# Optimization experiments

Measured on AMD Instinct MI355X. Metric: run time of the kernel, lower is better.

Reference implementation:

```python
import jax, jax.numpy as jnp
import numpy as np

N_EMBD = 1024
N_HEAD = 16

def setup_inputs() -> dict:
    key = jax.random.key(0)
    ks = jax.random.split(key, 5)
    B, T, C = 4, 2048, N_EMBD
    scale = 1.0 / np.sqrt(C)
    return {
        "x": jax.random.normal(ks[0], (B, T, C), dtype=jnp.float32),
        "w_qkv": jax.random.normal(ks[1], (C, 3 * C), dtype=jnp.float32) * scale,
        "b_qkv": jax.random.normal(ks[2], (3 * C,), dtype=jnp.float32) * 0.02,
        "w_proj": jax.random.normal(ks[3], (C, C), dtype=jnp.float32) * scale,
        "b_proj": jax.random.normal(ks[4], (C,), dtype=jnp.float32) * 0.02,
    }

def reference(x, w_qkv, b_qkv, w_proj, b_proj):
    B, T, C = x.shape
    H = N_HEAD
    D = C // H  # head dim
    qkv = x @ w_qkv + b_qkv  # [B,T,3C]
    q, k, v = jnp.split(qkv, 3, axis=-1)
    # [B,T,C] -> [B,H,T,D]
    q = q.reshape(B, T, H, D).transpose(0, 2, 1, 3)
    k = k.reshape(B, T, H, D).transpose(0, 2, 1, 3)
    v = v.reshape(B, T, H, D).transpose(0, 2, 1, 3)
    att = jnp.einsum("bhqd,bhkd->bhqk", q, k) / jnp.sqrt(jnp.asarray(D, x.dtype))
    causal = jnp.tril(jnp.ones((T, T), dtype=bool))  # [T,T]
    att = jnp.where(causal[None, None, :, :], att, -jnp.inf)
    att = jax.nn.softmax(att, axis=-1)
    y = jnp.einsum("bhqk,bhkd->bhqd", att, v)  # [B,H,T,D]
    y = y.transpose(0, 2, 1, 3).reshape(B, T, C)
    return y @ w_proj + b_proj
```

## Files before the change

### kernel.cpp

```cpp
#include <hip/hip_runtime.h>
#include <hip/hip_bf16.h>
#include <stdint.h>

typedef __bf16 bf16_8 __attribute__((ext_vector_type(8)));
typedef float f32_4 __attribute__((ext_vector_type(4)));
typedef short short4v __attribute__((ext_vector_type(4)));

#define VMCNT(n) asm volatile("s_waitcnt vmcnt(" #n ")" ::: "memory")
#define LGKM0 asm volatile("s_waitcnt lgkmcnt(0)" ::: "memory")
#define SBAR __builtin_amdgcn_s_barrier()
#define SCHB __builtin_amdgcn_sched_barrier(0)

static __device__ __forceinline__ unsigned short f2bf(float f) {
    union { float f; unsigned int u; } v; v.f = f;
    unsigned int u = v.u;
    unsigned int r = (u + 0x7fffu + ((u >> 16) & 1u)) >> 16;
    return (unsigned short)r;
}

static __device__ __forceinline__ unsigned int pack_bf16x2(float a, float b) {
    union { float f; unsigned int u; } ua, ub;
    ua.f = a; ub.f = b;
    return __builtin_amdgcn_perm(ub.u + 0x8000u, ua.u + 0x8000u, 0x07060302u);
}

static __device__ __forceinline__ f32_4 mfma_16x16x16_bf16(short4v a, short4v b, f32_4 c) {
#if __has_builtin(__builtin_amdgcn_mfma_f32_16x16x16bf16_1k)
    return __builtin_amdgcn_mfma_f32_16x16x16bf16_1k(a, b, c, 0, 0, 0);
#else
    asm volatile("v_mfma_f32_16x16x16_bf16 %0, %1, %2, %0"
                 : "+v"(c) : "v"(a), "v"(b));
    return c;
#endif
}

static __device__ __forceinline__ void gll16(const unsigned short* g, unsigned short* l) {
    __builtin_amdgcn_global_load_lds(
        (const __attribute__((address_space(1))) unsigned int*)g,
        (__attribute__((address_space(3))) unsigned int*)l, 16, 0, 0);
}

__global__ __launch_bounds__(256) void prep_kernel(
    const float* __restrict__ x, unsigned int* __restrict__ xbf,
    const float* __restrict__ w_qkv, unsigned short* __restrict__ wqkvt,
    const float* __restrict__ w_proj, unsigned short* __restrict__ wprojt) {
    __shared__ unsigned short tile[64][65];
    int bid = blockIdx.x;
    if (bid < 8192) {
        int i = bid * 256 + threadIdx.x;
        float4 f = ((const float4*)x)[i];
        uint2 o;
        o.x = pack_bf16x2(f.x, f.y);
        o.y = pack_bf16x2(f.z, f.w);
        ((uint2*)xbf)[i] = o;
        return;
    }
    const float* in; unsigned short* out; int N, bx, by;
    if (bid < 8960) {
        in = w_qkv; out = wqkvt; N = 3072;
        int t = bid - 8192; bx = t % 48; by = t / 48;
    } else {
        in = w_proj; out = wprojt; N = 1024;
        int t = bid - 8960; bx = t & 15; by = t >> 4;
    }
    const int K = 1024;
    int k0 = by * 64, n0 = bx * 64;
    int tc = threadIdx.x & 63, tr = threadIdx.x >> 6;
    for (int p = 0; p < 16; ++p) {
        int k = p * 4 + tr;
        tile[k][tc] = f2bf(in[(size_t)(k0 + k) * N + n0 + tc]);
    }
    __syncthreads();
    for (int p = 0; p < 16; ++p) {
        int n = p * 4 + tr;
        out[(size_t)(n0 + n) * K + k0 + tc] = tile[tc][n];
    }
}

#define QSCALE 0.1803368801111204f

__global__ __launch_bounds__(512) void gemm_qkv(
    const unsigned short* __restrict__ A,
    const unsigned short* __restrict__ Bt,
    const float* __restrict__ bias,
    int M, int N, int K,
    unsigned short* __restrict__ q_out, unsigned short* __restrict__ k_out,
    unsigned short* __restrict__ v_out) {
    __shared__ __align__(16) unsigned short As[3][256 * 64];
    __shared__ __align__(16) unsigned short Bs[3][128 * 64];
    int tid = threadIdx.x;
    int wave = tid >> 6, lane = tid & 63;
    int wm = wave >> 1, wn = wave & 1;
    int quad = lane >> 4, l16 = lane & 15;
    int m0 = blockIdx.y * 256, n0 = blockIdx.x * 128;
    int which = n0 >> 10;

    f32_4 acc[4][4] = {};

    int srow = lane >> 3;
    int scs = ((lane & 7) ^ srow) * 8;
    const unsigned short* Ag = A + (size_t)(m0 + wave * 32 + srow) * K + scs;
    const unsigned short* Bg = Bt + (size_t)(n0 + wave * 16 + srow) * K + scs;
    int sx = l16 & 7;

    unsigned short *a0 = As[0], *a1 = As[1], *a2 = As[2];
    unsigned short *b0 = Bs[0], *b1 = Bs[1], *b2 = Bs[2];

#define STG_A(dst, kc) do { \
        for (int g = 0; g < 4; ++g) \
            gll16(Ag + (kc) + (size_t)(g * 8) * K, (dst) + (wave * 32 + g * 8) * 64); \
    } while (0)
#define STG_B(dst, kc) do { \
        for (int g = 0; g < 2; ++g) \
            gll16(Bg + (kc) + (size_t)(g * 8) * K, (dst) + (wave * 16 + g * 8) * 64); \
    } while (0)

    STG_A(a0, 0); STG_B(b0, 0);
    STG_A(a1, 64); STG_B(b1, 64);

    const int nkt = K >> 6;
    for (int kt = 0; kt < nkt; ++kt) {
        if (kt + 1 < nkt) { VMCNT(6); } else { VMCNT(0); }
        SCHB; SBAR; SCHB;
        bf16_8 af[4], bfr[4];
        for (int i = 0; i < 4; ++i)
            af[i] = *(const bf16_8*)(a0 + (wm * 64 + i * 16 + l16) * 64 +
                                     ((unsigned)(quad ^ sx)) * 8);
        for (int j = 0; j < 4; ++j)
            bfr[j] = *(const bf16_8*)(b0 + (wn * 64 + j * 16 + l16) * 64 +
                                      ((unsigned)(quad ^ sx)) * 8);
        if (kt + 2 < nkt) STG_A(a2, (kt + 2) * 64);
        SCHB; SBAR; SCHB;
        LGKM0; SCHB;
        __builtin_amdgcn_s_setprio(1);
        if (which < 2) {
            for (int i = 0; i < 4; ++i)
                for (int j = 0; j < 4; ++j)
                    acc[i][j] = __builtin_amdgcn_mfma_f32_16x16x32_bf16(bfr[j], af[i], acc[i][j], 0, 0, 0);
        } else {
            for (int i = 0; i < 4; ++i)
                for (int j = 0; j < 4; ++j)
                    acc[i][j] = __builtin_amdgcn_mfma_f32_16x16x32_bf16(af[i], bfr[j], acc[i][j], 0, 0, 0);
        }
        __builtin_amdgcn_s_setprio(0);

        SCHB; SBAR; SCHB;
        for (int i = 0; i < 4; ++i)
            af[i] = *(const bf16_8*)(a0 + (wm * 64 + i * 16 + l16) * 64 +
                                     ((unsigned)((4 + quad) ^ sx)) * 8);
        for (int j = 0; j < 4; ++j)
            bfr[j] = *(const bf16_8*)(b0 + (wn * 64 + j * 16 + l16) * 64 +
                                      ((unsigned)((4 + quad) ^ sx)) * 8);
        if (kt + 2 < nkt) STG_B(b2, (kt + 2) * 64);
        SCHB; SBAR; SCHB;
        LGKM0; SCHB;
        __builtin_amdgcn_s_setprio(1);
        if (which < 2) {
            for (int i = 0; i < 4; ++i)
                for (int j = 0; j < 4; ++j)
                    acc[i][j] = __builtin_amdgcn_mfma_f32_16x16x32_bf16(bfr[j], af[i], acc[i][j], 0, 0, 0);
        } else {
            for (int i = 0; i < 4; ++i)
                for (int j = 0; j < 4; ++j)
                    acc[i][j] = __builtin_amdgcn_mfma_f32_16x16x32_bf16(af[i], bfr[j], acc[i][j], 0, 0, 0);
        }
        __builtin_amdgcn_s_setprio(0);

        unsigned short* t;
        t = a0; a0 = a1; a1 = a2; a2 = t;
        t = b0; b0 = b1; b1 = b2; b2 = t;
    }
#undef STG_A
#undef STG_B

    int b = m0 >> 11;
    int tbase = (m0 & 2047) + wm * 64;
    int nw0 = n0 + wn * 64;
    if (which < 2) {
        unsigned short* dst = which == 0 ? q_out : k_out;
        float scale = which == 0 ? QSCALE : 1.0f;
        int h0 = ((n0 & 1023) >> 6) + wn;
        size_t base = ((size_t)((b << 4) + h0) * 2048) * 64;
        for (int j = 0; j < 4; ++j) {
            float4 b4 = *(const float4*)(bias + nw0 + j * 16 + quad * 4);
            int d0 = j * 16 + quad * 4;
            for (int i = 0; i < 4; ++i) {
                int t = tbase + i * 16 + l16;
                uint2 pk;
                pk.x = pack_bf16x2((acc[i][j][0] + b4.x) * scale,
                                   (acc[i][j][1] + b4.y) * scale);
                pk.y = pack_bf16x2((acc[i][j][2] + b4.z) * scale,
                                   (acc[i][j][3] + b4.w) * scale);
                *(uint2*)(dst + base + (size_t)t * 64 + d0) = pk;
            }
        }
    } else {
        for (int j = 0; j < 4; ++j) {
            int n = nw0 + j * 16 + l16;
            int c = n & 1023, h = c >> 6, d = c & 63;
            float bs = bias[n];
            size_t base = ((size_t)((b << 4) + h) * 64 + d) * 2048;
            for (int i = 0; i < 4; ++i) {
                int t0 = tbase + i * 16 + quad * 4;
                uint2 pk;
                pk.x = pack_bf16x2(acc[i][j][0] + bs, acc[i][j][1] + bs);
                pk.y = pack_bf16x2(acc[i][j][2] + bs, acc[i][j][3] + bs);
                *(uint2*)(v_out + base + t0) = pk;
            }
        }
    }
}

__global__ __launch_bounds__(512) void gemm_proj(
    const unsigned short* __restrict__ A,
    const unsigned short* __restrict__ Bt,
    const float* __restrict__ bias,
    int M, int N, int K, float* __restrict__ outf) {
    __shared__ __align__(16) unsigned short As[3][256 * 64];
    __shared__ __align__(16) unsigned short Bs[3][128 * 64];
    int tid = threadIdx.x;
    int wave = tid >> 6, lane = tid & 63;
    int wm = wave >> 1, wn = wave & 1;
    int quad = lane >> 4, l16 = lane & 15;
    int m0 = blockIdx.y * 256, n0 = blockIdx.x * 128;

    f32_4 acc[4][4] = {};

    int srow = lane >> 3;
    int scs = ((lane & 7) ^ srow) * 8;
    const unsigned short* Ag = A + (size_t)(m0 + wave * 32 + srow) * K + scs;
    const unsigned short* Bg = Bt + (size_t)(n0 + wave * 16 + srow) * K + scs;
    int sx = l16 & 7;

    unsigned short *a0 = As[0], *a1 = As[1], *a2 = As[2];
    unsigned short *b0 = Bs[0], *b1 = Bs[1], *b2 = Bs[2];

#define STG_A(dst, kc) do { \
        for (int g = 0; g < 4; ++g) \
            gll16(Ag + (kc) + (size_t)(g * 8) * K, (dst) + (wave * 32 + g * 8) * 64); \
    } while (0)
#define STG_B(dst, kc) do { \
        for (int g = 0; g < 2; ++g) \
            gll16(Bg + (kc) + (size_t)(g * 8) * K, (dst) + (wave * 16 + g * 8) * 64); \
    } while (0)

    STG_A(a0, 0); STG_B(b0, 0);
    STG_A(a1, 64); STG_B(b1, 64);

    const int nkt = K >> 6;
    for (int kt = 0; kt < nkt; ++kt) {
        if (kt + 1 < nkt) { VMCNT(6); } else { VMCNT(0); }
        SCHB; SBAR; SCHB;
        bf16_8 af[4], bfr[4];
        for (int i = 0; i < 4; ++i)
            af[i] = *(const bf16_8*)(a0 + (wm * 64 + i * 16 + l16) * 64 +
                                     ((unsigned)(quad ^ sx)) * 8);
        for (int j = 0; j < 4; ++j)
            bfr[j] = *(const bf16_8*)(b0 + (wn * 64 + j * 16 + l16) * 64 +
                                      ((unsigned)(quad ^ sx)) * 8);
        if (kt + 2 < nkt) STG_A(a2, (kt + 2) * 64);
        SCHB; SBAR; SCHB;
        LGKM0; SCHB;
        __builtin_amdgcn_s_setprio(1);
        for (int i = 0; i < 4; ++i)
            for (int j = 0; j < 4; ++j)
                acc[i][j] = __builtin_amdgcn_mfma_f32_16x16x32_bf16(af[i], bfr[j], acc[i][j], 0, 0, 0);
        __builtin_amdgcn_s_setprio(0);

        SCHB; SBAR; SCHB;
        for (int i = 0; i < 4; ++i)
            af[i] = *(const bf16_8*)(a0 + (wm * 64 + i * 16 + l16) * 64 +
                                     ((unsigned)((4 + quad) ^ sx)) * 8);
        for (int j = 0; j < 4; ++j)
            bfr[j] = *(const bf16_8*)(b0 + (wn * 64 + j * 16 + l16) * 64 +
                                      ((unsigned)((4 + quad) ^ sx)) * 8);
        if (kt + 2 < nkt) STG_B(b2, (kt + 2) * 64);
        SCHB; SBAR; SCHB;
        LGKM0; SCHB;
        __builtin_amdgcn_s_setprio(1);
        for (int i = 0; i < 4; ++i)
            for (int j = 0; j < 4; ++j)
                acc[i][j] = __builtin_amdgcn_mfma_f32_16x16x32_bf16(af[i], bfr[j], acc[i][j], 0, 0, 0);
        __builtin_amdgcn_s_setprio(0);

        unsigned short* t;
        t = a0; a0 = a1; a1 = a2; a2 = t;
        t = b0; b0 = b1; b1 = b2; b2 = t;
    }
#undef STG_A
#undef STG_B

    for (int j = 0; j < 4; ++j) {
        int n = n0 + wn * 64 + j * 16 + l16;
        float bs = bias[n];
        for (int i = 0; i < 4; ++i) {
            int m = m0 + wm * 64 + i * 16 + quad * 4;
            for (int r = 0; r < 4; ++r)
                outf[(size_t)(m + r) * N + n] = acc[i][j][r] + bs;
        }
    }
}

__global__ __launch_bounds__(256, 5) void attn_kernel(
    const unsigned short* __restrict__ Q, const unsigned short* __restrict__ Kb,
    const unsigned short* __restrict__ Vt, unsigned short* __restrict__ Y,
    int T) {
    __shared__ __align__(16) unsigned short KsB[2][64 * 64];
    __shared__ __align__(16) unsigned short VtsB[2][64 * 64];

    int tid = threadIdx.x;
    int wave = tid >> 6, lane = tid & 63;
    int quad = lane >> 4, l16 = lane & 15;
    int bh = blockIdx.x;
    int b = bh >> 4, h = bh & 15;
    int qt = 31 - blockIdx.y;
    int qw = qt * 64 + wave * 16;
    int nkt = qt + 1;

    int srow = lane >> 3;
    int scs = ((lane & 7) ^ srow) * 8;
    int sx = l16 & 7;

    bf16_8 qa[2];
    for (int ks = 0; ks < 2; ++ks)
        qa[ks] = *(const bf16_8*)(Q + ((size_t)bh * T + qw + l16) * 64 + ks * 32 + quad * 8);

    f32_4 o[4] = {};
    f32_4 osum = {};
    short4v vones;
    { unsigned short one = 0x3F80;
      vones[0] = (short)one; vones[1] = (short)one; vones[2] = (short)one; vones[3] = (short)one; }

    for (int p = 0; p < 2; ++p) {
        int row = wave * 16 + p * 8;
        gll16(Kb + ((size_t)bh * T + row + srow) * 64 + scs, &KsB[0][row * 64]);
        gll16(Vt + ((size_t)bh * 64 + row + srow) * (size_t)T + scs, &VtsB[0][row * 64]);
    }
    __syncthreads();

    for (int kt = 0; kt < nkt; ++kt) {
        int cur = kt & 1;
        int kb = kt * 64;
        if (kt + 1 < nkt) {
            int kb2 = kb + 64, nxt = cur ^ 1;
            for (int p = 0; p < 2; ++p) {
                int row = wave * 16 + p * 8;
                gll16(Kb + ((size_t)bh * T + kb2 + row + srow) * 64 + scs, &KsB[nxt][row * 64]);
                gll16(Vt + ((size_t)bh * 64 + row + srow) * (size_t)T + kb2 + scs, &VtsB[nxt][row * 64]);
            }
        }
        const unsigned short* KsC = KsB[cur];
        const unsigned short* VtsC = VtsB[cur];

        f32_4 s[4] = {};
        for (int kf = 0; kf < 4; ++kf) {
            bf16_8 k0 = *(const bf16_8*)(KsC + (kf * 16 + l16) * 64 + ((unsigned)(quad ^ sx)) * 8);
            bf16_8 k1 = *(const bf16_8*)(KsC + (kf * 16 + l16) * 64 + ((unsigned)((4 + quad) ^ sx)) * 8);
            s[kf] = __builtin_amdgcn_mfma_f32_16x16x32_bf16(k0, qa[0], s[kf], 0, 0, 0);
            s[kf] = __builtin_amdgcn_mfma_f32_16x16x32_bf16(k1, qa[1], s[kf], 0, 0, 0);
        }

        if (kt == qt) {
            int q = qw + l16;
            for (int kf = 0; kf < 4; ++kf) {
                int kk = kb + kf * 16 + quad * 4;
                for (int r = 0; r < 4; ++r)
                    if (kk + r > q) s[kf][r] = -1e30f;
            }
        }

        short4v pb[4];
        for (int kf = 0; kf < 4; ++kf) {
            float p0 = __builtin_amdgcn_exp2f(s[kf][0]);
            float p1 = __builtin_amdgcn_exp2f(s[kf][1]);
            float p2 = __builtin_amdgcn_exp2f(s[kf][2]);
            float p3 = __builtin_amdgcn_exp2f(s[kf][3]);
            union { unsigned int u[2]; short4v s4; } pu;
            pu.u[0] = pack_bf16x2(p0, p1);
            pu.u[1] = pack_bf16x2(p2, p3);
            pb[kf] = pu.s4;
        }

        for (int kf = 0; kf < 4; ++kf) {
            osum = mfma_16x16x16_bf16(vones, pb[kf], osum);
            unsigned voff = ((unsigned)((2 * kf + (quad >> 1)) ^ sx)) * 8 + (quad & 1) * 4;
            for (int df = 0; df < 4; ++df) {
                short4v va = *(const short4v*)(VtsC + (df * 16 + l16) * 64 + voff);
                o[df] = mfma_16x16x16_bf16(va, pb[kf], o[df]);
            }
        }
        __syncthreads();
    }

    float inv = 1.0f / osum[0];
    unsigned short* yp = Y + ((size_t)b * T + qw + l16) * 1024 + h * 64 + quad * 4;
    for (int df = 0; df < 4; ++df) {
        uint2 pk;
        pk.x = pack_bf16x2(o[df][0] * inv, o[df][1] * inv);
        pk.y = pack_bf16x2(o[df][2] * inv, o[df][3] * inv);
        *(uint2*)(yp + df * 16) = pk;
    }
}

extern "C" void kernel_launch(void* const* d_in, const int* in_sizes, int n_in,
                              void* d_out, int out_size, void* d_ws, size_t ws_size,
                              hipStream_t stream) {
    const float* x = (const float*)d_in[0];
    const float* w_qkv = (const float*)d_in[1];
    const float* b_qkv = (const float*)d_in[2];
    const float* w_proj = (const float*)d_in[3];
    const float* b_proj = (const float*)d_in[4];
    float* out = (float*)d_out;

    unsigned short* xbf = (unsigned short*)d_ws;
    unsigned short* wqkvt = xbf + 8388608;
    unsigned short* wprojt = wqkvt + 3145728;
    unsigned short* Qb = wprojt + 1048576;
    unsigned short* Kb = Qb + 8388608;
    unsigned short* Vtb = Kb + 8388608;
    unsigned short* Yb = Vtb + 8388608;

    hipLaunchKernelGGL(prep_kernel, dim3(9216), dim3(256), 0, stream,
                       x, (unsigned int*)xbf, w_qkv, wqkvt, w_proj, wprojt);
    hipLaunchKernelGGL(gemm_qkv, dim3(24, 32), dim3(512), 0, stream,
                       xbf, wqkvt, b_qkv, 8192, 3072, 1024,
                       Qb, Kb, Vtb);
    hipLaunchKernelGGL(attn_kernel, dim3(64, 32), dim3(256), 0, stream,
                       Qb, Kb, Vtb, Yb, 2048);
    hipLaunchKernelGGL(gemm_proj, dim3(8, 32), dim3(512), 0, stream,
                       Yb, wprojt, b_proj, 8192, 1024, 1024, out);
}
```

Measured before the change: 262.1 us.

## Enlarge GEMM tiles to 256x256 with double-buffered LDS staging

Both the QKV and projection GEMMs move from 256x128 to 256x256 block tiles. The 8 waves are rearranged as 2x4, each owning 128x64 outputs with twice the accumulators. The three-stage LDS ring becomes a two-buffer scheme with a full vmcnt(0) wait each k-step, which gives up some load/compute overlap. Grids shrink to 384 and 128 blocks, so the projection GEMM under-fills 256 CUs, and higher register pressure may cut occupancy.

After: 501.0 us. +91.1%, slower.

```diff
diff --git a/kernel.cpp b/kernel.cpp
--- a/kernel.cpp
+++ b/kernel.cpp
@@ -86,52 +86,51 @@
     int M, int N, int K,
     unsigned short* __restrict__ q_out, unsigned short* __restrict__ k_out,
     unsigned short* __restrict__ v_out) {
-    __shared__ __align__(16) unsigned short As[3][256 * 64];
-    __shared__ __align__(16) unsigned short Bs[3][128 * 64];
+    __shared__ __align__(16) unsigned short As[2][256 * 64];
+    __shared__ __align__(16) unsigned short Bs[2][256 * 64];
     int tid = threadIdx.x;
     int wave = tid >> 6, lane = tid & 63;
-    int wm = wave >> 1, wn = wave & 1;
+    int wm = wave >> 2, wn = wave & 3;
     int quad = lane >> 4, l16 = lane & 15;
-    int m0 = blockIdx.y * 256, n0 = blockIdx.x * 128;
+    int m0 = blockIdx.y * 256, n0 = blockIdx.x * 256;
     int which = n0 >> 10;
 
-    f32_4 acc[4][4] = {};
+    f32_4 acc[8][4] = {};
 
     int srow = lane >> 3;
     int scs = ((lane & 7) ^ srow) * 8;
     const unsigned short* Ag = A + (size_t)(m0 + wave * 32 + srow) * K + scs;
-    const unsigned short* Bg = Bt + (size_t)(n0 + wave * 16 + srow) * K + scs;
+    const unsigned short* Bg = Bt + (size_t)(n0 + wave * 32 + srow) * K + scs;
     int sx = l16 & 7;
 
-    unsigned short *a0 = As[0], *a1 = As[1], *a2 = As[2];
-    unsigned short *b0 = Bs[0], *b1 = Bs[1], *b2 = Bs[2];
+    unsigned short *ac = As[0], *an = As[1];
+    unsigned short *bc = Bs[0], *bn = Bs[1];
 
 #define STG_A(dst, kc) do { \
         for (int g = 0; g < 4; ++g) \
             gll16(Ag + (kc) + (size_t)(g * 8) * K, (dst) + (wave * 32 + g * 8) * 64); \
     } while (0)
 #define STG_B(dst, kc) do { \
-        for (int g = 0; g < 2; ++g) \
-            gll16(Bg + (kc) + (size_t)(g * 8) * K, (dst) + (wave * 16 + g * 8) * 64); \
+        for (int g = 0; g < 4; ++g) \
+            gll16(Bg + (kc) + (size_t)(g * 8) * K, (dst) + (wave * 32 + g * 8) * 64); \
     } while (0)
 
-    STG_A(a0, 0); STG_B(b0, 0);
-    STG_A(a1, 64); STG_B(b1, 64);
+    STG_A(ac, 0); STG_B(bc, 0);
 
     const int nkt = K >> 6;
     for (int kt = 0; kt < nkt; ++kt) {
-        if (kt + 1 < nkt) { VMCNT(6); } else { VMCNT(0); }
-        SCHB; SBAR; SCHB;
+        int havenext = (kt + 1 < nkt);
+        VMCNT(0); SCHB; SBAR; SCHB;
+
         bf16_8 af[4], bfr[4];
-        for (int i = 0; i < 4; ++i)
-            af[i] = *(const bf16_8*)(a0 + (wm * 64 + i * 16 + l16) * 64 +
+        for (int j = 0; j < 4; ++j)
+            bfr[j] = *(const bf16_8*)(bc + (wn * 64 + j * 16 + l16) * 64 +
+                                      ((unsigned)(quad ^ sx)) * 8);
+        for (int i = 0; i < 4; ++i)
+            af[i] = *(const bf16_8*)(ac + (wm * 128 + i * 16 + l16) * 64 +
                                      ((unsigned)(quad ^ sx)) * 8);
-        for (int j = 0; j < 4; ++j)
-            bfr[j] = *(const bf16_8*)(b0 + (wn * 64 + j * 16 + l16) * 64 +
-                                      ((unsigned)(quad ^ sx)) * 8);
-        if (kt + 2 < nkt) STG_A(a2, (kt + 2) * 64);
-        SCHB; SBAR; SCHB;
-        LGKM0; SCHB;
+        if (havenext) STG_A(an, (kt + 1) * 64);
+        SCHB; SBAR; LGKM0; SCHB;
         __builtin_amdgcn_s_setprio(1);
         if (which < 2) {
             for (int i = 0; i < 4; ++i)
@@ -143,17 +142,33 @@
                     acc[i][j] = __builtin_amdgcn_mfma_f32_16x16x32_bf16(af[i], bfr[j], acc[i][j], 0, 0, 0);
         }
         __builtin_amdgcn_s_setprio(0);
-
-        SCHB; SBAR; SCHB;
-        for (int i = 0; i < 4; ++i)
-            af[i] = *(const bf16_8*)(a0 + (wm * 64 + i * 16 + l16) * 64 +
+        SCHB; SBAR; SCHB;
+
+        for (int i = 0; i < 4; ++i)
+            af[i] = *(const bf16_8*)(ac + (wm * 128 + (i + 4) * 16 + l16) * 64 +
+                                     ((unsigned)(quad ^ sx)) * 8);
+        if (havenext) STG_B(bn, (kt + 1) * 64);
+        SCHB; SBAR; LGKM0; SCHB;
+        __builtin_amdgcn_s_setprio(1);
+        if (which < 2) {
+            for (int i = 0; i < 4; ++i)
+                for (int j = 0; j < 4; ++j)
+                    acc[i + 4][j] = __builtin_amdgcn_mfma_f32_16x16x32_bf16(bfr[j], af[i], acc[i + 4][j], 0, 0, 0);
+        } else {
+            for (int i = 0; i < 4; ++i)
+                for (int j = 0; j < 4; ++j)
+                    acc[i + 4][j] = __builtin_amdgcn_mfma_f32_16x16x32_bf16(af[i], bfr[j], acc[i + 4][j], 0, 0, 0);
+        }
+        __builtin_amdgcn_s_setprio(0);
+        SCHB; SBAR; SCHB;
+
+        for (int j = 0; j < 4; ++j)
+            bfr[j] = *(const bf16_8*)(bc + (wn * 64 + j * 16 + l16) * 64 +
+                                      ((unsigned)((4 + quad) ^ sx)) * 8);
+        for (int i = 0; i < 4; ++i)
+            af[i] = *(const bf16_8*)(ac + (wm * 128 + i * 16 + l16) * 64 +
                                      ((unsigned)((4 + quad) ^ sx)) * 8);
-        for (int j = 0; j < 4; ++j)
-            bfr[j] = *(const bf16_8*)(b0 + (wn * 64 + j * 16 + l16) * 64 +
-                                      ((unsigned)((4 + quad) ^ sx)) * 8);
-        if (kt + 2 < nkt) STG_B(b2, (kt + 2) * 64);
-        SCHB; SBAR; SCHB;
-        LGKM0; SCHB;
+        SCHB; SBAR; LGKM0; SCHB;
         __builtin_amdgcn_s_setprio(1);
         if (which < 2) {
             for (int i = 0; i < 4; ++i)
@@ -165,16 +180,33 @@
                     acc[i][j] = __builtin_amdgcn_mfma_f32_16x16x32_bf16(af[i], bfr[j], acc[i][j], 0, 0, 0);
         }
         __builtin_amdgcn_s_setprio(0);
+        SCHB; SBAR; SCHB;
+
+        for (int i = 0; i < 4; ++i)
+            af[i] = *(const bf16_8*)(ac + (wm * 128 + (i + 4) * 16 + l16) * 64 +
+                                     ((unsigned)((4 + quad) ^ sx)) * 8);
+        SCHB; SBAR; LGKM0; SCHB;
+        __builtin_amdgcn_s_setprio(1);
+        if (which < 2) {
+            for (int i = 0; i < 4; ++i)
+                for (int j = 0; j < 4; ++j)
+                    acc[i + 4][j] = __builtin_amdgcn_mfma_f32_16x16x32_bf16(bfr[j], af[i], acc[i + 4][j], 0, 0, 0);
+        } else {
+            for (int i = 0; i < 4; ++i)
+                for (int j = 0; j < 4; ++j)
+                    acc[i + 4][j] = __builtin_amdgcn_mfma_f32_16x16x32_bf16(af[i], bfr[j], acc[i + 4][j], 0, 0, 0);
+        }
+        __builtin_amdgcn_s_setprio(0);
 
         unsigned short* t;
-        t = a0; a0 = a1; a1 = a2; a2 = t;
-        t = b0; b0 = b1; b1 = b2; b2 = t;
+        t = ac; ac = an; an = t;
+        t = bc; bc = bn; bn = t;
     }
 #undef STG_A
 #undef STG_B
 
     int b = m0 >> 11;
-    int tbase = (m0 & 2047) + wm * 64;
+    int tbase = (m0 & 2047) + wm * 128;
     int nw0 = n0 + wn * 64;
     if (which < 2) {
         unsigned short* dst = which == 0 ? q_out : k_out;
@@ -184,7 +216,7 @@
         for (int j = 0; j < 4; ++j) {
             float4 b4 = *(const float4*)(bias + nw0 + j * 16 + quad * 4);
             int d0 = j * 16 + quad * 4;
-            for (int i = 0; i < 4; ++i) {
+            for (int i = 0; i < 8; ++i) {
                 int t = tbase + i * 16 + l16;
                 uint2 pk;
                 pk.x = pack_bf16x2((acc[i][j][0] + b4.x) * scale,
@@ -200,7 +232,7 @@
             int c = n & 1023, h = c >> 6, d = c & 63;
             float bs = bias[n];
             size_t base = ((size_t)((b << 4) + h) * 64 + d) * 2048;
-            for (int i = 0; i < 4; ++i) {
+            for (int i = 0; i < 8; ++i) {
                 int t0 = tbase + i * 16 + quad * 4;
                 uint2 pk;
                 pk.x = pack_bf16x2(acc[i][j][0] + bs, acc[i][j][1] + bs);
@@ -216,76 +248,93 @@
     const unsigned short* __restrict__ Bt,
     const float* __restrict__ bias,
     int M, int N, int K, float* __restrict__ outf) {
-    __shared__ __align__(16) unsigned short As[3][256 * 64];
-    __shared__ __align__(16) unsigned short Bs[3][128 * 64];
+    __shared__ __align__(16) unsigned short As[2][256 * 64];
+    __shared__ __align__(16) unsigned short Bs[2][256 * 64];
     int tid = threadIdx.x;
     int wave = tid >> 6, lane = tid & 63;
-    int wm = wave >> 1, wn = wave & 1;
+    int wm = wave >> 2, wn = wave & 3;
     int quad = lane >> 4, l16 = lane & 15;
-    int m0 = blockIdx.y * 256, n0 = blockIdx.x * 128;
-
-    f32_4 acc[4][4] = {};
+    int m0 = blockIdx.y * 256, n0 = blockIdx.x * 256;
+
+    f32_4 acc[8][4] = {};
 
     int srow = lane >> 3;
     int scs = ((lane & 7) ^ srow) * 8;
     const unsigned short* Ag = A + (size_t)(m0 + wave * 32 + srow) * K + scs;
-    const unsigned short* Bg = Bt + (size_t)(n0 + wave * 16 + srow) * K + scs;
+    const unsigned short* Bg = Bt + (size_t)(n0 + wave * 32 + srow) * K + scs;
     int sx = l16 & 7;
 
-    unsigned short *a0 = As[0], *a1 = As[1], *a2 = As[2];
-    unsigned short *b0 = Bs[0], *b1 = Bs[1], *b2 = Bs[2];
+    unsigned short *ac = As[0], *an = As[1];
+    unsigned short *bc = Bs[0], *bn = Bs[1];
 
 #define STG_A(dst, kc) do { \
         for (int g = 0; g < 4; ++g) \
             gll16(Ag + (kc) + (size_t)(g * 8) * K, (dst) + (wave * 32 + g * 8) * 64); \
     } while (0)
 #define STG_B(dst, kc) do { \
-        for (int g = 0; g < 2; ++g) \
-            gll16(Bg + (kc) + (size_t)(g * 8) * K, (dst) + (wave * 16 + g * 8) * 64); \
+        for (int g = 0; g < 4; ++g) \
+            gll16(Bg + (kc) + (size_t)(g * 8) * K, (dst) + (wave * 32 + g * 8) * 64); \
     } while (0)
 
-    STG_A(a0, 0); STG_B(b0, 0);
-    STG_A(a1, 64); STG_B(b1, 64);
+    STG_A(ac, 0); STG_B(bc, 0);
 
     const int nkt = K >> 6;
     for (int kt = 0; kt < nkt; ++kt) {
-        if (kt + 1 < nkt) { VMCNT(6); } else { VMCNT(0); }
-        SCHB; SBAR; SCHB;
+        int havenext = (kt + 1 < nkt);
+        VMCNT(0); SCHB; SBAR; SCHB;
+
         bf16_8 af[4], bfr[4];
-        for (int i = 0; i < 4; ++i)
-            af[i] = *(const bf16_8*)(a0 + (wm * 64 + i * 16 + l16) * 64 +
+        for (int j = 0; j < 4; ++j)
+            bfr[j] = *(const bf16_8*)(bc + (wn * 64 + j * 16 + l16) * 64 +
+                                      ((unsigned)(quad ^ sx)) * 8);
+        for (int i = 0; i < 4; ++i)
+            af[i] = *(const bf16_8*)(ac + (wm * 128 + i * 16 + l16) * 64 +
                                      ((unsigned)(quad ^ sx)) * 8);
-        for (int j = 0; j < 4; ++j)
-            bfr[j] = *(const bf16_8*)(b0 + (wn * 64 + j * 16 + l16) * 64 +
-                                      ((unsigned)(quad ^ sx)) * 8);
-        if (kt + 2 < nkt) STG_A(a2, (kt + 2) * 64);
-        SCHB; SBAR; SCHB;
-        LGKM0; SCHB;
+        if (havenext) STG_A(an, (kt + 1) * 64);
+        SCHB; SBAR; LGKM0; SCHB;
         __builtin_amdgcn_s_setprio(1);
         for (int i = 0; i < 4; ++i)
             for (int j = 0; j < 4; ++j)
                 acc[i][j] = __builtin_amdgcn_mfma_f32_16x16x32_bf16(af[i], bfr[j], acc[i][j], 0, 0, 0);
         __builtin_amdgcn_s_setprio(0);
-
-        SCHB; SBAR; SCHB;
-        for (int i = 0; i < 4; ++i)
-            af[i] = *(const bf16_8*)(a0 + (wm * 64 + i * 16 + l16) * 64 +
+        SCHB; SBAR; SCHB;
+        for (int i = 0; i < 4; ++i)
+            af[i] = *(const bf16_8*)(ac + (wm * 128 + (i + 4) * 16 + l16) * 64 +
+                                     ((unsigned)(quad ^ sx)) * 8);
+        if (havenext) STG_B(bn, (kt + 1) * 64);
+        SCHB; SBAR; LGKM0; SCHB;
+        __builtin_amdgcn_s_setprio(1);
+        for (int i = 0; i < 4; ++i)
+            for (int j = 0; j < 4; ++j)
+                acc[i + 4][j] = __builtin_amdgcn_mfma_f32_16x16x32_bf16(af[i], bfr[j], acc[i + 4][j], 0, 0, 0);
+        __builtin_amdgcn_s_setprio(0);
+        SCHB; SBAR; SCHB;
+        for (int j = 0; j < 4; ++j)
+            bfr[j] = *(const bf16_8*)(bc + (wn * 64 + j * 16 + l16) * 64 +
+                                      ((unsigned)((4 + quad) ^ sx)) * 8);
+        for (int i = 0; i < 4; ++i)
+            af[i] = *(const bf16_8*)(ac + (wm * 128 + i * 16 + l16) * 64 +
                                      ((unsigned)((4 + quad) ^ sx)) * 8);
-        for (int j = 0; j < 4; ++j)
-            bfr[j] = *(const bf16_8*)(b0 + (wn * 64 + j * 16 + l16) * 64 +
-                                      ((unsigned)((4 + quad) ^ sx)) * 8);
-        if (kt + 2 < nkt) STG_B(b2, (kt + 2) * 64);
-        SCHB; SBAR; SCHB;
-        LGKM0; SCHB;
+        SCHB; SBAR; LGKM0; SCHB;
         __builtin_amdgcn_s_setprio(1);
         for (int i = 0; i < 4; ++i)
             for (int j = 0; j < 4; ++j)
                 acc[i][j] = __builtin_amdgcn_mfma_f32_16x16x32_bf16(af[i], bfr[j], acc[i][j], 0, 0, 0);
         __builtin_amdgcn_s_setprio(0);
+        SCHB; SBAR; SCHB;
+        for (int i = 0; i < 4; ++i)
+            af[i] = *(const bf16_8*)(ac + (wm * 128 + (i + 4) * 16 + l16) * 64 +
+                                     ((unsigned)((4 + quad) ^ sx)) * 8);
+        SCHB; SBAR; LGKM0; SCHB;
+        __builtin_amdgcn_s_setprio(1);
+        for (int i = 0; i < 4; ++i)
+            for (int j = 0; j < 4; ++j)
+                acc[i + 4][j] = __builtin_amdgcn_mfma_f32_16x16x32_bf16(af[i], bfr[j], acc[i + 4][j], 0, 0, 0);
+        __builtin_amdgcn_s_setprio(0);
 
         unsigned short* t;
-        t = a0; a0 = a1; a1 = a2; a2 = t;
-        t = b0; b0 = b1; b1 = b2; b2 = t;
+        t = ac; ac = an; an = t;
+        t = bc; bc = bn; bn = t;
     }
 #undef STG_A
 #undef STG_B
@@ -293,8 +342,8 @@
     for (int j = 0; j < 4; ++j) {
         int n = n0 + wn * 64 + j * 16 + l16;
         float bs = bias[n];
-        for (int i = 0; i < 4; ++i) {
-            int m = m0 + wm * 64 + i * 16 + quad * 4;
+        for (int i = 0; i < 8; ++i) {
+            int m = m0 + wm * 128 + i * 16 + quad * 4;
             for (int r = 0; r < 4; ++r)
                 outf[(size_t)(m + r) * N + n] = acc[i][j][r] + bs;
         }
@@ -422,11 +471,11 @@
 
     hipLaunchKernelGGL(prep_kernel, dim3(9216), dim3(256), 0, stream,
                        x, (unsigned int*)xbf, w_qkv, wqkvt, w_proj, wprojt);
-    hipLaunchKernelGGL(gemm_qkv, dim3(24, 32), dim3(512), 0, stream,
+    hipLaunchKernelGGL(gemm_qkv, dim3(12, 32), dim3(512), 0, stream,
                        xbf, wqkvt, b_qkv, 8192, 3072, 1024,
                        Qb, Kb, Vtb);
     hipLaunchKernelGGL(attn_kernel, dim3(64, 32), dim3(256), 0, stream,
                        Qb, Kb, Vtb, Yb, 2048);
-    hipLaunchKernelGGL(gemm_proj, dim3(8, 32), dim3(512), 0, stream,
+    hipLaunchKernelGGL(gemm_proj, dim3(4, 32), dim3(512), 0, stream,
                        Yb, wprojt, b_proj, 8192, 1024, 1024, out);
 }
```

## Shrink proj GEMM to 128x128 tiles with simple double buffering

Applied to the files above, without the earlier changes.

The projection GEMM moves from 256x128 tiles with 512 threads and a triple-buffered, split-phase pipeline to 128x128 tiles with 256 threads, plain double buffering and one __syncthreads per K step. The grid doubles to 512 blocks, which is meant to fill the GPU better for this small GEMM (256 blocks before). In exchange it loses the fine-grained barrier and priority scheduling that overlapped loads with MFMA, and there is no explicit vmcnt wait before the sync, so the async LDS loads may not be ordered correctly.

After: 245.5 us. -6.3%, faster.

```diff
diff --git a/kernel.cpp b/kernel.cpp
--- a/kernel.cpp
+++ b/kernel.cpp
@@ -78,6 +78,7 @@
 }
 
 #define QSCALE 0.1803368801111204f
+#define BK 64
 
 __global__ __launch_bounds__(512) void gemm_qkv(
     const unsigned short* __restrict__ A,
@@ -211,84 +212,62 @@
     }
 }
 
-__global__ __launch_bounds__(512) void gemm_proj(
+__global__ __launch_bounds__(256) void gemm_proj(
     const unsigned short* __restrict__ A,
     const unsigned short* __restrict__ Bt,
     const float* __restrict__ bias,
     int M, int N, int K, float* __restrict__ outf) {
-    __shared__ __align__(16) unsigned short As[3][256 * 64];
-    __shared__ __align__(16) unsigned short Bs[3][128 * 64];
+    __shared__ __align__(16) unsigned short As[2][128 * BK];
+    __shared__ __align__(16) unsigned short Bs[2][128 * BK];
     int tid = threadIdx.x;
     int wave = tid >> 6, lane = tid & 63;
-    int wm = wave >> 1, wn = wave & 1;
+    int wm = wave & 1, wn = wave >> 1;
     int quad = lane >> 4, l16 = lane & 15;
-    int m0 = blockIdx.y * 256, n0 = blockIdx.x * 128;
+    int m0 = blockIdx.y * 128, n0 = blockIdx.x * 128;
 
     f32_4 acc[4][4] = {};
 
     int srow = lane >> 3;
     int scs = ((lane & 7) ^ srow) * 8;
     const unsigned short* Ag = A + (size_t)(m0 + wave * 32 + srow) * K + scs;
-    const unsigned short* Bg = Bt + (size_t)(n0 + wave * 16 + srow) * K + scs;
+    const unsigned short* Bg = Bt + (size_t)(n0 + wave * 32 + srow) * K + scs;
+    int sbase = wave * 32 * BK;
     int sx = l16 & 7;
 
-    unsigned short *a0 = As[0], *a1 = As[1], *a2 = As[2];
-    unsigned short *b0 = Bs[0], *b1 = Bs[1], *b2 = Bs[2];
-
-#define STG_A(dst, kc) do { \
-        for (int g = 0; g < 4; ++g) \
-            gll16(Ag + (kc) + (size_t)(g * 8) * K, (dst) + (wave * 32 + g * 8) * 64); \
-    } while (0)
-#define STG_B(dst, kc) do { \
-        for (int g = 0; g < 2; ++g) \
-            gll16(Bg + (kc) + (size_t)(g * 8) * K, (dst) + (wave * 16 + g * 8) * 64); \
-    } while (0)
-
-    STG_A(a0, 0); STG_B(b0, 0);
-    STG_A(a1, 64); STG_B(b1, 64);
-
-    const int nkt = K >> 6;
-    for (int kt = 0; kt < nkt; ++kt) {
-        if (kt + 1 < nkt) { VMCNT(6); } else { VMCNT(0); }
-        SCHB; SBAR; SCHB;
-        bf16_8 af[4], bfr[4];
+    for (int p = 0; p < 4; ++p) {
+        gll16(Ag + (size_t)(8 * p) * K, As[0] + sbase + p * 8 * BK);
+        gll16(Bg + (size_t)(8 * p) * K, Bs[0] + sbase + p * 8 * BK);
+    }
+    __syncthreads();
+
+    int cur = 0;
+    for (int kt = 0; kt < K; kt += BK) {
+        if (kt + BK < K) {
+            int nxt = cur ^ 1;
+            for (int p = 0; p < 4; ++p) {
+                gll16(Ag + kt + BK + (size_t)(8 * p) * K, As[nxt] + sbase + p * 8 * BK);
+                gll16(Bg + kt + BK + (size_t)(8 * p) * K, Bs[nxt] + sbase + p * 8 * BK);
+            }
+        }
+        const unsigned short* Ac = As[cur];
+        const unsigned short* Bc = Bs[cur];
+        bf16_8 af[4][2], bfr[4][2];
         for (int i = 0; i < 4; ++i)
-            af[i] = *(const bf16_8*)(a0 + (wm * 64 + i * 16 + l16) * 64 +
-                                     ((unsigned)(quad ^ sx)) * 8);
+            for (int ks = 0; ks < 2; ++ks)
+                af[i][ks] = *(const bf16_8*)(Ac + (wm * 64 + i * 16 + l16) * BK +
+                                             ((unsigned)((ks * 4 + quad) ^ sx)) * 8);
         for (int j = 0; j < 4; ++j)
-            bfr[j] = *(const bf16_8*)(b0 + (wn * 64 + j * 16 + l16) * 64 +
-                                      ((unsigned)(quad ^ sx)) * 8);
-        if (kt + 2 < nkt) STG_A(a2, (kt + 2) * 64);
-        SCHB; SBAR; SCHB;
-        LGKM0; SCHB;
-        __builtin_amdgcn_s_setprio(1);
+            for (int ks = 0; ks < 2; ++ks)
+                bfr[j][ks] = *(const bf16_8*)(Bc + (wn * 64 + j * 16 + l16) * BK +
+                                              ((unsigned)((ks * 4 + quad) ^ sx)) * 8);
         for (int i = 0; i < 4; ++i)
-            for (int j = 0; j < 4; ++j)
-                acc[i][j] = __builtin_amdgcn_mfma_f32_16x16x32_bf16(af[i], bfr[j], acc[i][j], 0, 0, 0);
-        __builtin_amdgcn_s_setprio(0);
-
-        SCHB; SBAR; SCHB;
-        for (int i = 0; i < 4; ++i)
-            af[i] = *(const bf16_8*)(a0 + (wm * 64 + i * 16 + l16) * 64 +
-                                     ((unsigned)((4 + quad) ^ sx)) * 8);
-        for (int j = 0; j < 4; ++j)
-            bfr[j] = *(const bf16_8*)(b0 + (wn * 64 + j * 16 + l16) * 64 +
-                                      ((unsigned)((4 + quad) ^ sx)) * 8);
-        if (kt + 2 < nkt) STG_B(b2, (kt + 2) * 64);
-        SCHB; SBAR; SCHB;
-        LGKM0; SCHB;
-        __builtin_amdgcn_s_setprio(1);
-        for (int i = 0; i < 4; ++i)
-            for (int j = 0; j < 4; ++j)
-                acc[i][j] = __builtin_amdgcn_mfma_f32_16x16x32_bf16(af[i], bfr[j], acc[i][j], 0, 0, 0);
-        __builtin_amdgcn_s_setprio(0);
-
-        unsigned short* t;
-        t = a0; a0 = a1; a1 = a2; a2 = t;
-        t = b0; b0 = b1; b1 = b2; b2 = t;
-    }
-#undef STG_A
-#undef STG_B
+            for (int j = 0; j < 4; ++j) {
+                acc[i][j] = __builtin_amdgcn_mfma_f32_16x16x32_bf16(af[i][0], bfr[j][0], acc[i][j], 0, 0, 0);
+                acc[i][j] = __builtin_amdgcn_mfma_f32_16x16x32_bf16(af[i][1], bfr[j][1], acc[i][j], 0, 0, 0);
+            }
+        __syncthreads();
+        cur ^= 1;
+    }
 
     for (int j = 0; j < 4; ++j) {
         int n = n0 + wn * 64 + j * 16 + l16;
@@ -427,6 +406,6 @@
                        Qb, Kb, Vtb);
     hipLaunchKernelGGL(attn_kernel, dim3(64, 32), dim3(256), 0, stream,
                        Qb, Kb, Vtb, Yb, 2048);
-    hipLaunchKernelGGL(gemm_proj, dim3(8, 32), dim3(512), 0, stream,
+    hipLaunchKernelGGL(gemm_proj, dim3(8, 64), dim3(256), 0, stream,
                        Yb, wprojt, b_proj, 8192, 1024, 1024, out);
 }
```
